# Optimization experiments

Hardware: AMD Instinct MI355X
Metric: run time of the kernel (lower is better)

The kernel has to match this reference:

```python
import jax, jax.numpy as jnp
import numpy as np


def conv2d(x, w, b=None):
    # 3x3, stride 1, pad 1, NCHW/OIHW
    y = jax.lax.conv_general_dilated(x, w, (1, 1), ((1, 1), (1, 1)),
                                     dimension_numbers=('NCHW', 'OIHW', 'NCHW'))
    return y if b is None else y + b[None, :, None, None]


def maxpool3s2(x):
    # MaxPool2d(kernel_size=3, stride=2, padding=1)
    return jax.lax.reduce_window(x, -jnp.inf, jax.lax.max,
                                 (1, 1, 3, 3), (1, 1, 2, 2),
                                 ((0, 0), (0, 0), (1, 1), (1, 1)))


def up2(x):
    # F.interpolate(scale_factor=2, mode='bilinear', align_corners=False)
    N, C, H, W = x.shape
    return jax.image.resize(x, (N, C, 2 * H, 2 * W), method='bilinear')


def deform_conv2d(x, offset, w, dg):
    # mmcv-style DeformConv2d (no modulation, no bias), 3x3, pad 1, stride 1.
    # offset: (N, dg*2*9, H, W) -> (N, dg, 9, (y,x), H, W)
    N, Cin, H, W = x.shape
    Cout = w.shape[0]
    K, pad = 9, 1
    Cg = Cin // dg
    off = offset.reshape(N, dg, K, 2, H, W)
    ky, kx = jnp.meshgrid(jnp.arange(3), jnp.arange(3), indexing='ij')
    kdy = (ky.reshape(K) - pad).astype(x.dtype)
    kdx = (kx.reshape(K) - pad).astype(x.dtype)
    gy = jnp.arange(H, dtype=x.dtype)
    gx = jnp.arange(W, dtype=x.dtype)
    py = off[:, :, :, 0] + gy[None, None, None, :, None] + kdy[None, None, :, None, None]
    px = off[:, :, :, 1] + gx[None, None, None, None, :] + kdx[None, None, :, None, None]
    y0f = jnp.floor(py)
    x0f = jnp.floor(px)
    wy = (py - y0f).reshape(N, dg, 1, K * H * W)
    wx = (px - x0f).reshape(N, dg, 1, K * H * W)
    y0 = y0f.astype(jnp.int32)
    x0 = x0f.astype(jnp.int32)
    xg = x.reshape(N, dg, Cg, H * W)

    def gather(yi, xi):
        valid = ((yi >= 0) & (yi < H) & (xi >= 0) & (xi < W))
        idx = (jnp.clip(yi, 0, H - 1) * W + jnp.clip(xi, 0, W - 1)).reshape(N, dg, 1, K * H * W)
        v = jnp.take_along_axis(xg, idx, axis=-1)  # (N, dg, Cg, K*H*W)
        return v * valid.reshape(N, dg, 1, K * H * W).astype(x.dtype)

    v00 = gather(y0, x0)
    v01 = gather(y0, x0 + 1)
    v10 = gather(y0 + 1, x0)
    v11 = gather(y0 + 1, x0 + 1)
    col = (v00 * (1 - wy) * (1 - wx) + v01 * (1 - wy) * wx
           + v10 * wy * (1 - wx) + v11 * wy * wx)
    col = col.reshape(N, Cin, K, H, W)  # im2col with bilinear sampling
    return jnp.einsum('ock,nckhw->nohw', w.reshape(Cout, Cin, K), col)


def pyramid(img, blocks):
    feats = []
    x = img
    for w1, b1, w2, b2 in blocks:
        x = jax.nn.relu(conv2d(x, w1, b1))
        x = jax.nn.relu(conv2d(x, w2, b2))
        x = maxpool3s2(x)
        feats.append(x)
    return feats


def _forward(ref_image, unreg_image,
             fe0_w1, fe0_b1, fe0_w2, fe0_b2,
             fe1_w1, fe1_b1, fe1_w2, fe1_b2,
             fe2_w1, fe2_b1, fe2_w2, fe2_b2,
             ob0_w, ob0_b, ob1_w, ob1_b, ob2_w, ob2_b,
             og0_w, og0_b, og1_w, og1_b, og2_w, og2_b,
             dc0_w, dc1_w, dc2_w,
             fc0_w, fc0_b, fc1_w, fc1_b, fc2_w, fc2_b,
             dob_w, dob_b, dog_w, dog_b, ddc_w):
    relu = jax.nn.relu
    blocks = [(fe0_w1, fe0_b1, fe0_w2, fe0_b2),
              (fe1_w1, fe1_b1, fe1_w2, fe1_b2),
              (fe2_w1, fe2_b1, fe2_w2, fe2_b2)]
    rf = pyramid(ref_image, blocks)
    uf = pyramid(unreg_image, blocks)
    ob = [(ob0_w, ob0_b), (ob1_w, ob1_b), (ob2_w, ob2_b)]
    og = [(og0_w, og0_b), (og1_w, og1_b), (og2_w, og2_b)]
    dc = [dc0_w, dc1_w, dc2_w]
    fc = [(fc0_w, fc0_b), (fc1_w, fc1_b), (fc2_w, fc2_b)]
    offs = [None] * 3
    feats = [None] * 3
    for i in range(2, -1, -1):  # coarse to fine
        o = relu(conv2d(jnp.concatenate([rf[i], uf[i]], axis=1), *ob[i]))
        inp = o if i == 2 else jnp.concatenate([o, up2(offs[i + 1])], axis=1)
        offs[i] = relu(conv2d(inp, *og[i]))  # 18-channel offsets
        f = relu(deform_conv2d(uf[i], offs[i], dc[i], 1))
        finp = f if i == 2 else jnp.concatenate([f, up2(feats[i + 1])], axis=1)
        feats[i] = relu(conv2d(finp, *fc[i]))
    do = conv2d(jnp.concatenate([rf[0], feats[0]], axis=1), dob_w, dob_b)
    do = conv2d(jnp.concatenate([do, offs[0]], axis=1), dog_w, dog_b)  # 36-ch offsets
    return deform_conv2d(feats[0], do, ddc_w, 2)  # (N, 2, H/2, W/2)


def setup_inputs() -> dict:
    key = jax.random.key(0)
    ks = iter(jax.random.split(key, 48))
    IC = 16

    def W(cout, cin):
        return jax.random.normal(next(ks), (cout, cin, 3, 3), jnp.float32) / np.sqrt(cin * 9.0)

    def B(c):
        return jax.random.normal(next(ks), (c,), jnp.float32) * 0.01

    d = {
        'ref_image': jax.random.normal(next(ks), (4, 1, 512, 512), jnp.float32),
        'unreg_image': jax.random.normal(next(ks), (4, 1, 512, 512), jnp.float32),
        'fe0_w1': W(IC, 1), 'fe0_b1': B(IC), 'fe0_w2': W(IC, IC), 'fe0_b2': B(IC),
        'fe1_w1': W(IC, IC), 'fe1_b1': B(IC), 'fe1_w2': W(IC, IC), 'fe1_b2': B(IC),
        'fe2_w1': W(IC, IC), 'fe2_b1': B(IC), 'fe2_w2': W(IC, IC), 'fe2_b2': B(IC),
        'ob0_w': W(IC, 2 * IC), 'ob0_b': B(IC),
        'ob1_w': W(IC, 2 * IC), 'ob1_b': B(IC),
        'ob2_w': W(IC, 2 * IC), 'ob2_b': B(IC),
        'og0_w': W(18, IC + 18), 'og0_b': B(18),
        'og1_w': W(18, IC + 18), 'og1_b': B(18),
        'og2_w': W(18, IC), 'og2_b': B(18),
        'dc0_w': W(IC, IC), 'dc1_w': W(IC, IC), 'dc2_w': W(IC, IC),
        'fc0_w': W(IC, 2 * IC), 'fc0_b': B(IC),
        'fc1_w': W(IC, 2 * IC), 'fc1_b': B(IC),
        'fc2_w': W(IC, IC), 'fc2_b': B(IC),
        'dob_w': W(IC, 2 * IC), 'dob_b': B(IC),
        'dog_w': W(36, IC + 18), 'dog_b': B(36),
        'ddc_w': W(2, IC),
    }
    return d


def reference(ref_image, unreg_image,
              fe0_w1, fe0_b1, fe0_w2, fe0_b2,
              fe1_w1, fe1_b1, fe1_w2, fe1_b2,
              fe2_w1, fe2_b1, fe2_w2, fe2_b2,
              ob0_w, ob0_b, ob1_w, ob1_b, ob2_w, ob2_b,
              og0_w, og0_b, og1_w, og1_b, og2_w, og2_b,
              dc0_w, dc1_w, dc2_w,
              fc0_w, fc0_b, fc1_w, fc1_b, fc2_w, fc2_b,
              dob_w, dob_b, dog_w, dog_b, ddc_w):
    return _forward(ref_image, unreg_image,
                    fe0_w1, fe0_b1, fe0_w2, fe0_b2,
                    fe1_w1, fe1_b1, fe1_w2, fe1_b2,
                    fe2_w1, fe2_b1, fe2_w2, fe2_b2,
                    ob0_w, ob0_b, ob1_w, ob1_b, ob2_w, ob2_b,
                    og0_w, og0_b, og1_w, og1_b, og2_w, og2_b,
                    dc0_w, dc1_w, dc2_w,
                    fc0_w, fc0_b, fc1_w, fc1_b, fc2_w, fc2_b,
                    dob_w, dob_b, dog_w, dog_b, ddc_w)
```

## Files before the change

kernel.cpp:

```cpp
#include <hip/hip_runtime.h>
#include <math.h>

typedef _Float16 half2_t __attribute__((ext_vector_type(2)));
typedef _Float16 half8 __attribute__((ext_vector_type(8)));
typedef float floatx4 __attribute__((ext_vector_type(4)));

__device__ __forceinline__ unsigned packh2(float a, float b) {
  half2_t h;
  h.x = (_Float16)a;
  h.y = (_Float16)b;
  return __builtin_bit_cast(unsigned, h);
}
__device__ __forceinline__ unsigned short f2h(float a) {
  return __builtin_bit_cast(unsigned short, (_Float16)a);
}
__device__ __forceinline__ float h2f(unsigned short u) {
  return (float)__builtin_bit_cast(_Float16, u);
}
__device__ __forceinline__ float dot2acc(unsigned a, unsigned b, float c) {
  half2_t ha = __builtin_bit_cast(half2_t, a);
  half2_t hb = __builtin_bit_cast(half2_t, b);
#if __has_builtin(__builtin_amdgcn_fdot2)
  return __builtin_amdgcn_fdot2(ha, hb, c, false);
#else
  c = fmaf((float)ha.x, (float)hb.x, c);
  return fmaf((float)ha.y, (float)hb.y, c);
#endif
}
__device__ __forceinline__ half8 splat8(_Float16 x) {
  half8 r;
#pragma unroll
  for (int j = 0; j < 8; ++j) r[j] = x;
  return r;
}

__global__ __launch_bounds__(256) void wdcpair_k(
    const float* __restrict__ a, const float* __restrict__ b,
    const float* __restrict__ c, const float* __restrict__ d,
    unsigned* __restrict__ out) {
  int t = blockIdx.x * 256 + threadIdx.x;
  if (t < 3456) {
    int conv = t / 1152, r = t % 1152;
    int k = r / 128, cp = (r / 16) % 8, o = r & 15;
    const float* w = conv == 0 ? a : (conv == 1 ? b : c);
    out[t] = packh2(w[(o * 16 + 2 * cp) * 9 + k], w[(o * 16 + 2 * cp + 1) * 9 + k]);
  } else if (t < 3600) {
    int r = t - 3456;
    int o = r & 1, jp = (r >> 1) & 3, g = (r >> 3) & 1, k = r >> 4;
    out[t] = packh2(d[(o * 16 + g * 8 + 2 * jp) * 9 + k],
                    d[(o * 16 + g * 8 + 2 * jp + 1) * 9 + k]);
  }
}

__global__ __launch_bounds__(256) void wmfma_k(
    const float* __restrict__ w0, const float* __restrict__ w1,
    const float* __restrict__ w2, const float* __restrict__ w3,
    const float* __restrict__ w4, const float* __restrict__ w5,
    unsigned short* __restrict__ out) {
  int t = blockIdx.x * 256 + threadIdx.x;
  if (t >= 15360) return;
  int conv = t / 2560, r = t % 2560;
  int c = r / 512, L = (r / 8) % 64, j = r & 7;
  int quad = L >> 4, o = L & 15;
  int k = 32 * c + quad * 8 + j;
  int tap = k >> 4, cin = k & 15;
  float v;
  if (conv == 5) {
    v = (tap < 9 && cin == 0) ? w5[o * 9 + tap] : 0.f;
  } else {
    const float* w = conv == 0 ? w0 : conv == 1 ? w1 : conv == 2 ? w2 : conv == 3 ? w3 : w4;
    v = (tap < 9) ? w[((size_t)o * 16 + cin) * 9 + tap] : 0.f;
  }
  out[t] = f2h(v);
}

struct W32Entry { const float* src; int cin; };
struct W32Table { W32Entry e[8]; };
__global__ __launch_bounds__(256) void wmfma32_k(W32Table t, unsigned short* __restrict__ out) {
  int i = blockIdx.x * 256 + threadIdx.x;
  if (i >= 7 * 4608) return;
  int conv = i / 4608, r = i % 4608;
  int tap = r / 512, L = (r / 8) % 64, j = r & 7;
  int quad = L >> 4, o = L & 15;
  int c = quad * 8 + j;
  W32Entry en = t.e[conv];
  float v = (c < en.cin) ? en.src[((size_t)o * en.cin + c) * 9 + tap] : 0.f;
  out[i] = f2h(v);
}

struct SPEntry { const float* src; int cin; int cout; int ct; int dstoff; };
struct SPTable { SPEntry e[4]; };
__global__ __launch_bounds__(256) void wsplit_k(SPTable t, unsigned short* __restrict__ out) {
  SPEntry en = t.e[blockIdx.y];
  int aSize = en.ct * 2560;
  int bSize = (en.cin > 16) ? en.ct * 4608 : 0;
  int i = blockIdx.x * 256 + threadIdx.x;
  if (i >= aSize + bSize) return;
  float v;
  if (i < aSize) {
    int ct = i / 2560, r = i % 2560;
    int c = r / 512, L = (r / 8) % 64, j = r & 7;
    int quad = L >> 4, o16 = L & 15;
    int k = 32 * c + quad * 8 + j;
    int tap = k >> 4, cin = k & 15;
    int o = ct * 16 + o16;
    v = (tap < 9 && o < en.cout) ? en.src[((size_t)o * en.cin + cin) * 9 + tap] : 0.f;
  } else {
    int r2 = i - aSize;
    int ct = r2 / 4608, r = r2 % 4608;
    int tap = r / 512, L = (r / 8) % 64, j = r & 7;
    int quad = L >> 4, o16 = L & 15;
    int cin = quad * 8 + j;
    int o = ct * 16 + o16;
    v = (cin < en.cin - 16 && o < en.cout)
            ? en.src[((size_t)o * en.cin + 16 + cin) * 9 + tap] : 0.f;
  }
  out[en.dstoff + i] = f2h(v);
}

__device__ __forceinline__ void conv_mfma(
    const unsigned short* __restrict__ src, int SW,
    unsigned short* __restrict__ dst, int DPS, const half8* __restrict__ bf,
    const float* __restrict__ bias, int POS, int OW, int tid, int relu,
    int domask, int gby, int gbx, int bound) {
  const int lane = tid & 63, wid = tid >> 6;
  const int quad = lane >> 4, m = lane & 15;
  const int tap01 = quad >> 1, cin8 = (quad & 1) * 8;
  const int ntiles = (POS + 15) >> 4;
  float bs = bias[m];
  half8 zero;
#pragma unroll
  for (int j = 0; j < 8; ++j) zero[j] = (_Float16)0;
  for (int T = wid; T < ntiles; T += 4) {
    int pa = T * 16 + m;
    pa = pa < POS ? pa : POS - 1;
    int ya = pa / OW, xa = pa - ya * OW;
    floatx4 acc = {0.f, 0.f, 0.f, 0.f};
#pragma unroll
    for (int c = 0; c < 5; ++c) {
      int tap = 2 * c + tap01;
      half8 a = zero;
      if (tap < 9) {
        int dy = tap / 3, dx = tap - (tap / 3) * 3;
        a = *(const half8*)(src + ((ya + dy) * SW + xa + dx) * 16 + cin8);
      }
      acc = __builtin_amdgcn_mfma_f32_16x16x32_f16(a, bf[c], acc, 0, 0, 0);
    }
#pragma unroll
    for (int r = 0; r < 4; ++r) {
      int pd = T * 16 + quad * 4 + r;
      if (pd < POS) {
        float v = acc[r] + bs;
        if (relu) v = fmaxf(v, 0.f);
        if (domask) {
          int yd = pd / OW, xd = pd - (pd / OW) * OW;
          int gy = gby + yd, gx = gbx + xd;
          if (gy < 0 || gy >= bound || gx < 0 || gx >= bound) v = 0.f;
        }
        dst[pd * DPS + m] = f2h(v);
      }
    }
  }
}

__device__ __forceinline__ void conv_mfma32(
    const unsigned short* __restrict__ src, int SW,
    unsigned short* __restrict__ dst, int DPS, const half8* __restrict__ bf,
    const float* __restrict__ bias, int POS, int OW, int tid, int relu,
    int domask, int gby, int gbx, int bound) {
  const int lane = tid & 63, wid = tid >> 6;
  const int quad = lane >> 4, m = lane & 15;
  const int ntiles = (POS + 15) >> 4;
  float bs = bias[m];
  for (int T = wid; T < ntiles; T += 4) {
    int pa = T * 16 + m;
    pa = pa < POS ? pa : POS - 1;
    int ya = pa / OW, xa = pa - ya * OW;
    floatx4 acc = {0.f, 0.f, 0.f, 0.f};
#pragma unroll
    for (int tap = 0; tap < 9; ++tap) {
      int dy = tap / 3, dx = tap - (tap / 3) * 3;
      half8 a = *(const half8*)(src + ((ya + dy) * SW + xa + dx) * 32 + quad * 8);
      acc = __builtin_amdgcn_mfma_f32_16x16x32_f16(a, bf[tap], acc, 0, 0, 0);
    }
#pragma unroll
    for (int r = 0; r < 4; ++r) {
      int pd = T * 16 + quad * 4 + r;
      if (pd < POS) {
        float v = acc[r] + bs;
        if (relu) v = fmaxf(v, 0.f);
        if (domask) {
          int yd = pd / OW, xd = pd - (pd / OW) * OW;
          int gy = gby + yd, gx = gbx + xd;
          if (gy < 0 || gy >= bound || gx < 0 || gx >= bound) v = 0.f;
        }
        dst[pd * DPS + m] = f2h(v);
      }
    }
  }
}

template <int CT, int HASB, int NT>
__device__ __forceinline__ void conv_split_mfma(
    const unsigned short* __restrict__ srcB, const unsigned short* __restrict__ srcO,
    const unsigned short* __restrict__ wbase, float* __restrict__ outLds, int OSTRIDE,
    const float* __restrict__ bias, int NOUT, int relu, int tid) {
  const int lane = tid & 63, wid = tid >> 6;
  const int quad = lane >> 4, m = lane & 15;
  const int tap01 = quad >> 1, cin8 = (quad & 1) * 8;
  half8 zero;
#pragma unroll
  for (int j = 0; j < 8; ++j) zero[j] = (_Float16)0;
  floatx4 acc[CT][NT];
#pragma unroll
  for (int ct = 0; ct < CT; ++ct)
#pragma unroll
    for (int t = 0; t < NT; ++t) acc[ct][t] = floatx4{0.f, 0.f, 0.f, 0.f};
#pragma unroll
  for (int ct = 0; ct < CT; ++ct) {
    half8 bfA[5];
#pragma unroll
    for (int c = 0; c < 5; ++c)
      bfA[c] = *(const half8*)(wbase + ((ct * 5 + c) * 64 + lane) * 8);
#pragma unroll
    for (int t = 0; t < NT; ++t) {
      int pa = (wid + 4 * t) * 16 + m;
      int ya = pa >> 4, xa = pa & 15;
#pragma unroll
      for (int c = 0; c < 5; ++c) {
        int tap = 2 * c + tap01;
        half8 a = zero;
        if (tap < 9) {
          int dy = tap / 3, dx = tap - (tap / 3) * 3;
          a = *(const half8*)(srcB + ((ya + dy) * 18 + xa + dx) * 18 + cin8);
        }
        acc[ct][t] = __builtin_amdgcn_mfma_f32_16x16x32_f16(a, bfA[c], acc[ct][t], 0, 0, 0);
      }
    }
  }
  if (HASB) {
    const unsigned short* wb = wbase + CT * 2560;
#pragma unroll
    for (int ct = 0; ct < CT; ++ct) {
      half8 bfB[9];
#pragma unroll
      for (int c = 0; c < 9; ++c)
        bfB[c] = *(const half8*)(wb + ((ct * 9 + c) * 64 + lane) * 8);
#pragma unroll
      for (int t = 0; t < NT; ++t) {
        int pa = (wid + 4 * t) * 16 + m;
        int ya = pa >> 4, xa = pa & 15;
#pragma unroll
        for (int tap = 0; tap < 9; ++tap) {
          int dy = tap / 3, dx = tap - (tap / 3) * 3;
          half8 a = *(const half8*)(srcO + ((ya + dy) * 18 + xa + dx) * 34 + quad * 8);
          acc[ct][t] = __builtin_amdgcn_mfma_f32_16x16x32_f16(a, bfB[tap], acc[ct][t], 0, 0, 0);
        }
      }
    }
  }
  __syncthreads();
#pragma unroll
  for (int ct = 0; ct < CT; ++ct) {
    int o = ct * 16 + m;
#pragma unroll
    for (int t = 0; t < NT; ++t) {
#pragma unroll
      for (int r = 0; r < 4; ++r) {
        int pd = (wid + 4 * t) * 16 + quad * 4 + r;
        if (o < NOUT) {
          float v = acc[ct][t][r] + bias[o];
          if (relu) v = fmaxf(v, 0.f);
          outLds[pd * OSTRIDE + o] = v;
        }
      }
    }
  }
}

__global__ __launch_bounds__(256) void fe0_fused_k(
    const float* __restrict__ refI, const float* __restrict__ unrI,
    const unsigned short* __restrict__ wm1, const float* __restrict__ b1,
    const unsigned short* __restrict__ wm2, const float* __restrict__ b2,
    float* __restrict__ outR, float* __restrict__ outU,
    unsigned short* __restrict__ outRH, unsigned short* __restrict__ outUH) {
  __shared__ __attribute__((aligned(16))) unsigned short bufA[441 * 16];
  __shared__ __attribute__((aligned(16))) unsigned short c1h[361 * 16];
  const int z = blockIdx.z;
  const int im = z >> 2, n = z & 3;
  const float* img = (im ? unrI : refI) + (size_t)n * 512 * 512;
  float* outp = (im ? outU : outR) + (size_t)n * 16 * 256 * 256;
  unsigned short* outh = (im ? outUH : outRH) + (size_t)n * 256 * 256 * 16;
  const int py0 = blockIdx.y * 8, px0 = blockIdx.x * 8;
  const int tid = threadIdx.x;

  half8 bf1[5], bf2[5];
  {
    const int lane = tid & 63;
#pragma unroll
    for (int c = 0; c < 5; ++c) {
      bf1[c] = *(const half8*)(wm1 + (c * 64 + lane) * 8);
      bf2[c] = *(const half8*)(wm2 + (c * 64 + lane) * 8);
    }
  }

  {
    unsigned* s32 = (unsigned*)bufA;
    for (int i = tid; i < 441; i += 256) {
      int yi = i / 21, xi = i - yi * 21;
      int gy = 2 * py0 - 3 + yi, gx = 2 * px0 - 3 + xi;
      float v = 0.f;
      if (gy >= 0 && gy < 512 && gx >= 0 && gx < 512) v = img[gy * 512 + gx];
      uint4 q0 = {packh2(v, 0.f), 0u, 0u, 0u};
      uint4 q1 = {0u, 0u, 0u, 0u};
      *(uint4*)(s32 + i * 8) = q0;
      *(uint4*)(s32 + i * 8 + 4) = q1;
    }
  }
  __syncthreads();

  conv_mfma(bufA, 21, c1h, 16, bf1, b1, 361, 19, tid, 1, 1, 2 * py0 - 2, 2 * px0 - 2, 512);
  __syncthreads();
  conv_mfma(c1h, 19, bufA, 18, bf2, b2, 289, 17, tid, 1, 0, 0, 0, 0);
  __syncthreads();

  unsigned short* stage = c1h;
  for (int i = tid; i < 1024; i += 256) {
    int c = i & 15, r = i >> 4;
    int py = r >> 3, px = r & 7;
    unsigned short m = 0;
#pragma unroll
    for (int dy = 0; dy < 3; ++dy) {
      int gy = 2 * (py0 + py) - 1 + dy;
      if (gy < 0 || gy >= 512) continue;
#pragma unroll
      for (int dx = 0; dx < 3; ++dx) {
        int gx = 2 * (px0 + px) - 1 + dx;
        if (gx < 0 || gx >= 512) continue;
        unsigned short v = bufA[((2 * py + dy) * 17 + 2 * px + dx) * 18 + c];
        m = (v > m) ? v : m;
      }
    }
    stage[r * 18 + c] = m;
  }
  __syncthreads();

  for (int i = tid; i < 1024; i += 256) {
    int c = i >> 6, r = i & 63, py = r >> 3, px = r & 7;
    unsigned short hb = stage[r * 18 + c];
    outp[((size_t)c * 256 + py0 + py) * 256 + px0 + px] = h2f(hb);
    outh[(((size_t)(py0 + py)) * 256 + px0 + px) * 16 + c] = hb;
  }
}

__global__ __launch_bounds__(256) void fe12_fused_k(
    const float* __restrict__ in,
    const unsigned short* __restrict__ wm1, const float* __restrict__ b1,
    const unsigned short* __restrict__ wm2, const float* __restrict__ b2,
    float* __restrict__ outC, unsigned short* __restrict__ outHWC, int Hin) {
  __shared__ __attribute__((aligned(16))) unsigned short inh[441 * 16];
  __shared__ __attribute__((aligned(16))) unsigned short c1h[361 * 16];
  const int n = blockIdx.z;
  const int Ho = Hin >> 1;
  const int py0 = blockIdx.y * 8, px0 = blockIdx.x * 8;
  const int tid = threadIdx.x;
  const float* inN = in + (size_t)n * 16 * Hin * Hin;
  const size_t HH = (size_t)Hin * Hin;

  half8 bf1[5], bf2[5];
  {
    const int lane = tid & 63;
#pragma unroll
    for (int c = 0; c < 5; ++c) {
      bf1[c] = *(const half8*)(wm1 + (c * 64 + lane) * 8);
      bf2[c] = *(const half8*)(wm2 + (c * 64 + lane) * 8);
    }
  }

  unsigned* inh32 = (unsigned*)inh;
  for (int i = tid; i < 8 * 441; i += 256) {
    int cp = i / 441, r = i - cp * 441;
    int yi = r / 21, xi = r - yi * 21;
    int gy = 2 * py0 - 3 + yi, gx = 2 * px0 - 3 + xi;
    float v0 = 0.f, v1 = 0.f;
    if (gy >= 0 && gy < Hin && gx >= 0 && gx < Hin) {
      const float* s = inN + (size_t)(2 * cp) * HH + (size_t)gy * Hin + gx;
      v0 = s[0];
      v1 = s[HH];
    }
    inh32[r * 8 + cp] = packh2(v0, v1);
  }
  __syncthreads();

  conv_mfma(inh, 21, c1h, 16, bf1, b1, 361, 19, tid, 1, 1, 2 * py0 - 2, 2 * px0 - 2, Hin);
  __syncthreads();
  conv_mfma(c1h, 19, inh, 18, bf2, b2, 289, 17, tid, 1, 0, 0, 0, 0);
  __syncthreads();

  unsigned short* stage = c1h;
  for (int i = tid; i < 1024; i += 256) {
    int c = i & 15, r = i >> 4;
    int py = r >> 3, px = r & 7;
    unsigned short m = 0;
#pragma unroll
    for (int dy = 0; dy < 3; ++dy) {
      int gy = 2 * (py0 + py) - 1 + dy;
      if (gy < 0 || gy >= Hin) continue;
#pragma unroll
      for (int dx = 0; dx < 3; ++dx) {
        int gx = 2 * (px0 + px) - 1 + dx;
        if (gx < 0 || gx >= Hin) continue;
        unsigned short v = inh[((2 * py + dy) * 17 + 2 * px + dx) * 18 + c];
        m = (v > m) ? v : m;
      }
    }
    stage[r * 18 + c] = m;
  }
  __syncthreads();

  float* outp = outC + (size_t)n * 16 * Ho * Ho;
  for (int i = tid; i < 1024; i += 256) {
    int c = i >> 6, r = i & 63, py = r >> 3, px = r & 7;
    unsigned short hb = stage[r * 18 + c];
    outp[((size_t)c * Ho + py0 + py) * Ho + px0 + px] = h2f(hb);
    if (n >= 4)
      outHWC[(((size_t)(n - 4) * Ho + py0 + py) * Ho + px0 + px) * 16 + c] = hb;
  }
}

template <int HAS_UP>
__global__ __launch_bounds__(256) void obog_k(
    const float* __restrict__ rf, const float* __restrict__ uf,
    const unsigned short* __restrict__ offsUp,
    const unsigned short* __restrict__ wmob, const float* __restrict__ bob,
    const unsigned short* __restrict__ wog, const float* __restrict__ bog,
    unsigned short* __restrict__ offsOut, int H) {
  __shared__ __attribute__((aligned(16))) unsigned POOL[5460];
  const int n = blockIdx.z;
  const int bx = blockIdx.x * 16, by = blockIdx.y * 8;
  const int tid = threadIdx.x;
  const size_t HH = (size_t)H * H;
  const float* r0 = rf + (size_t)n * 16 * HH;
  const float* u0 = uf + (size_t)n * 16 * HH;

  for (int i = tid; i < 3840; i += 256) {
    int cp = i / 240, r = i - cp * 240;
    int ly = r / 20, lx = r - ly * 20;
    int gy = by + ly - 2, gx = bx + lx - 2;
    float v0 = 0.f, v1 = 0.f;
    if (gy >= 0 && gy < H && gx >= 0 && gx < H) {
      const float* s = (cp < 8) ? r0 + (size_t)(2 * cp) * HH : u0 + (size_t)(2 * cp - 16) * HH;
      size_t off = (size_t)gy * H + gx;
      v0 = s[off];
      v1 = s[HH + off];
    }
    POOL[r * 16 + cp] = packh2(v0, v1);
  }
  __syncthreads();

  {
    half8 bf[9];
    const int lane = tid & 63;
#pragma unroll
    for (int c = 0; c < 9; ++c) bf[c] = *(const half8*)(wmob + (c * 64 + lane) * 8);
    conv_mfma32((const unsigned short*)POOL, 20, (unsigned short*)(POOL + 3840), 18,
                bf, bob, 180, 18, tid, 1, 1, by - 1, bx - 1, H);
  }
  __syncthreads();

  if (HAS_UP) {
    const int H2 = H >> 1;
    const unsigned short* os = offsUp + (size_t)n * 18 * H2 * H2;
    for (int i = tid; i < 16 * 180; i += 256) {
      int cp = i / 180, r = i - cp * 180;
      unsigned val = 0u;
      if (cp < 9) {
        int y1 = r / 18, x1 = r - y1 * 18;
        int gy = by + y1 - 1, gx = bx + x1 - 1;
        if (gy >= 0 && gy < H && gx >= 0 && gx < H) {
          float sy = 0.5f * gy - 0.25f, sx = 0.5f * gx - 0.25f;
          float y0f = floorf(sy), x0f = floorf(sx);
          float wy = sy - y0f, wx = sx - x0f;
          int y0 = (int)y0f, x0 = (int)x0f;
          int y0c = min(max(y0, 0), H2 - 1), y1c = min(max(y0 + 1, 0), H2 - 1);
          int x0c = min(max(x0, 0), H2 - 1), x1c = min(max(x0 + 1, 0), H2 - 1);
          const unsigned short* sp = os + (size_t)(2 * cp) * H2 * H2;
          float v0 = (1.f - wy) * ((1.f - wx) * h2f(sp[y0c * H2 + x0c]) + wx * h2f(sp[y0c * H2 + x1c])) +
                     wy * ((1.f - wx) * h2f(sp[y1c * H2 + x0c]) + wx * h2f(sp[y1c * H2 + x1c]));
          sp += (size_t)H2 * H2;
          float v1 = (1.f - wy) * ((1.f - wx) * h2f(sp[y0c * H2 + x0c]) + wx * h2f(sp[y0c * H2 + x1c])) +
                     wy * ((1.f - wx) * h2f(sp[y1c * H2 + x0c]) + wx * h2f(sp[y1c * H2 + x1c]));
          val = packh2(v0, v1);
        }
      }
      POOL[r * 17 + cp] = val;
    }
    __syncthreads();
  }

  conv_split_mfma<2, HAS_UP, 2>((const unsigned short*)(POOL + 3840),
                                (const unsigned short*)POOL, wog,
                                (float*)POOL, 19, bog, 18, 1, tid);
  __syncthreads();

  {
    int pix = tid & 127, half = tid >> 7;
    const float* of = (const float*)POOL + (size_t)pix * 19 + half * 9;
    int ty = pix >> 4, tx = pix & 15;
    unsigned short* op = offsOut + (size_t)n * 18 * HH + (size_t)(half * 9) * HH +
                         (size_t)(by + ty) * H + (bx + tx);
#pragma unroll
    for (int o = 0; o < 9; ++o) op[(size_t)o * HH] = f2h(of[o]);
  }
}

template <int HAS_UP>
__global__ __launch_bounds__(256) void defc_k(
    const unsigned short* __restrict__ ufHWC, const unsigned short* __restrict__ offs,
    const unsigned* __restrict__ wdc2, const float* __restrict__ featsUp,
    const unsigned short* __restrict__ wmfc, const float* __restrict__ bfc,
    float* __restrict__ featsOut, unsigned short* __restrict__ outHwc, int H) {
  __shared__ __attribute__((aligned(16))) unsigned ldsC[180 * 17];
  const int n = blockIdx.z;
  const int bx = blockIdx.x * 16, by = blockIdx.y * 8;
  const int tid = threadIdx.x;
  const size_t HH = (size_t)H * H;
  const unsigned short* inN = ufHWC + (size_t)n * HH * 16;
  const unsigned short* offN = offs + (size_t)n * 18 * HH;

  half8 bf[9];
  {
    const int lane = tid & 63;
#pragma unroll
    for (int c = 0; c < 9; ++c) bf[c] = *(const half8*)(wmfc + (c * 64 + lane) * 8);
  }

  for (int p = tid; p < 180; p += 256) {
    int y1 = p / 18, x1 = p - y1 * 18;
    int h = by + y1 - 1, w = bx + x1 - 1;
    bool valid = (h >= 0 && h < H && w >= 0 && w < H);
    float acc[16];
#pragma unroll
    for (int o = 0; o < 16; ++o) acc[o] = 0.f;
    if (valid) {
      size_t hw = (size_t)h * H + w;
#pragma unroll
      for (int k = 0; k < 9; ++k) {
        int ky = k / 3 - 1, kx = k % 3 - 1;
        float oy = h2f(offN[(size_t)(2 * k) * HH + hw]);
        float ox = h2f(offN[(size_t)(2 * k + 1) * HH + hw]);
        float py = (float)(h + ky) + oy;
        float px = (float)(w + kx) + ox;
        float y0f = floorf(py), x0f = floorf(px);
        float fy = py - y0f, fx = px - x0f;
        int y0 = (int)y0f, x0 = (int)x0f;
        bool vy0 = ((unsigned)y0 < (unsigned)H);
        bool vy1 = ((unsigned)(y0 + 1) < (unsigned)H);
        bool vx0 = ((unsigned)x0 < (unsigned)H);
        bool vx1 = ((unsigned)(x0 + 1) < (unsigned)H);
        int y0c = min(max(y0, 0), H - 1), y1c = min(max(y0 + 1, 0), H - 1);
        int x0c = min(max(x0, 0), H - 1), x1c = min(max(x0 + 1, 0), H - 1);
        float w00 = (vy0 && vx0) ? (1.f - fy) * (1.f - fx) : 0.f;
        float w01 = (vy0 && vx1) ? (1.f - fy) * fx : 0.f;
        float w10 = (vy1 && vx0) ? fy * (1.f - fx) : 0.f;
        float w11 = (vy1 && vx1) ? fy * fx : 0.f;
        half8 s00 = splat8((_Float16)w00);
        half8 s01 = splat8((_Float16)w01);
        half8 s10 = splat8((_Float16)w10);
        half8 s11 = splat8((_Float16)w11);
        const unsigned short* p00 = inN + ((size_t)y0c * H + x0c) * 16;
        const unsigned short* p01 = inN + ((size_t)y0c * H + x1c) * 16;
        const unsigned short* p10 = inN + ((size_t)y1c * H + x0c) * 16;
        const unsigned short* p11 = inN + ((size_t)y1c * H + x1c) * 16;
        const unsigned* wk2 = wdc2 + k * 128;
#pragma unroll
        for (int c8 = 0; c8 < 2; ++c8) {
          half8 a00 = *(const half8*)(p00 + c8 * 8);
          half8 a01 = *(const half8*)(p01 + c8 * 8);
          half8 a10 = *(const half8*)(p10 + c8 * 8);
          half8 a11 = *(const half8*)(p11 + c8 * 8);
          half8 vb = a00 * s00 + a01 * s01 + a10 * s10 + a11 * s11;
          uint4 vp = __builtin_bit_cast(uint4, vb);
          unsigned vpa[4] = {vp.x, vp.y, vp.z, vp.w};
#pragma unroll
          for (int jp = 0; jp < 4; ++jp) {
            const unsigned* wrow = wk2 + (c8 * 4 + jp) * 16;
#pragma unroll
            for (int o = 0; o < 16; ++o)
              acc[o] = dot2acc(vpa[jp], wrow[o], acc[o]);
          }
        }
      }
    }
#pragma unroll
    for (int cc = 0; cc < 8; ++cc) {
      float a0 = valid ? fmaxf(acc[2 * cc], 0.f) : 0.f;
      float a1 = valid ? fmaxf(acc[2 * cc + 1], 0.f) : 0.f;
      ldsC[p * 17 + cc] = packh2(a0, a1);
      if (!HAS_UP) ldsC[p * 17 + 8 + cc] = 0u;
    }
  }

  if (HAS_UP) {
    const int H2 = H >> 1;
    const float* fu = featsUp + (size_t)n * 16 * H2 * H2;
    for (int i = tid; i < 8 * 180; i += 256) {
      int cp = i / 180, r = i - cp * 180;
      int y1 = r / 18, x1 = r - y1 * 18;
      int gy = by + y1 - 1, gx = bx + x1 - 1;
      float v0 = 0.f, v1 = 0.f;
      if (gy >= 0 && gy < H && gx >= 0 && gx < H) {
        float sy = 0.5f * gy - 0.25f, sx = 0.5f * gx - 0.25f;
        float y0f = floorf(sy), x0f = floorf(sx);
        float wy = sy - y0f, wx = sx - x0f;
        int y0 = (int)y0f, x0 = (int)x0f;
        int y0c = min(max(y0, 0), H2 - 1), y1c = min(max(y0 + 1, 0), H2 - 1);
        int x0c = min(max(x0, 0), H2 - 1), x1c = min(max(x0 + 1, 0), H2 - 1);
        const float* sp = fu + (size_t)(2 * cp) * H2 * H2;
        v0 = (1.f - wy) * ((1.f - wx) * sp[y0c * H2 + x0c] + wx * sp[y0c * H2 + x1c]) +
             wy * ((1.f - wx) * sp[y1c * H2 + x0c] + wx * sp[y1c * H2 + x1c]);
        sp += (size_t)H2 * H2;
        v1 = (1.f - wy) * ((1.f - wx) * sp[y0c * H2 + x0c] + wx * sp[y0c * H2 + x1c]) +
             wy * ((1.f - wx) * sp[y1c * H2 + x0c] + wx * sp[y1c * H2 + x1c]);
      }
      ldsC[r * 17 + 8 + cp] = packh2(v0, v1);
    }
  }
  __syncthreads();

  {
    const int lane = tid & 63, wid = tid >> 6;
    const int quad = lane >> 4, m = lane & 15;
    const unsigned short* src = (const unsigned short*)ldsC;
    float bs = bfc[m];
    for (int T = wid; T < 8; T += 4) {
      int pa = T * 16 + m;
      int ya = pa >> 4, xa = pa & 15;
      floatx4 acc = {0.f, 0.f, 0.f, 0.f};
#pragma unroll
      for (int tap = 0; tap < 9; ++tap) {
        int dy = tap / 3, dx = tap - (tap / 3) * 3;
        half8 a = *(const half8*)(src + ((ya + dy) * 18 + xa + dx) * 34 + quad * 8);
        acc = __builtin_amdgcn_mfma_f32_16x16x32_f16(a, bf[tap], acc, 0, 0, 0);
      }
#pragma unroll
      for (int r = 0; r < 4; ++r) {
        int pd = T * 16 + quad * 4 + r;
        int yd = pd >> 4, xd = pd & 15;
        float v = fmaxf(acc[r] + bs, 0.f);
        if (featsOut)
          featsOut[(size_t)n * 16 * HH + (size_t)m * HH + (size_t)(by + yd) * H + bx + xd] = v;
        if (outHwc)
          outHwc[((size_t)n * HH + (size_t)(by + yd) * H + bx + xd) * 16 + m] = f2h(v);
      }
    }
  }
}

__global__ __launch_bounds__(256) void final_k(
    const unsigned short* __restrict__ rfh, const unsigned short* __restrict__ f0hwc,
    const unsigned short* __restrict__ offs0,
    const unsigned short* __restrict__ wmdob, const float* __restrict__ bdob,
    const unsigned short* __restrict__ wdog, const float* __restrict__ bdog,
    const unsigned* __restrict__ wddc2, float* __restrict__ out) {
  __shared__ __attribute__((aligned(16))) unsigned POOL[9472];
  const int H = 256;
  const size_t HH = 65536;
  const int n = blockIdx.z;
  const int bx = blockIdx.x * 16, by = blockIdx.y * 16;
  const int tid = threadIdx.x;
  const unsigned short* r0h = rfh + (size_t)n * HH * 16;
  const unsigned short* f0h = f0hwc + (size_t)n * HH * 16;

  for (int i = tid; i < 6400; i += 256) {
    int cp = i / 400, r = i - cp * 400;
    int ly = r / 20, lx = r - ly * 20;
    int gy = by + ly - 2, gx = bx + lx - 2;
    unsigned val = 0u;
    if (gy >= 0 && gy < H && gx >= 0 && gx < H) {
      const unsigned short* base = (cp < 8) ? r0h : f0h;
      int ch = (cp < 8) ? 2 * cp : 2 * cp - 16;
      val = *(const unsigned*)(base + ((size_t)gy * H + gx) * 16 + ch);
    }
    POOL[r * 16 + cp] = val;
  }
  __syncthreads();

  {
    half8 bf[9];
    const int lane = tid & 63;
#pragma unroll
    for (int c = 0; c < 9; ++c) bf[c] = *(const half8*)(wmdob + (c * 64 + lane) * 8);
    conv_mfma32((const unsigned short*)POOL, 20, (unsigned short*)(POOL + 6400), 18,
                bf, bdob, 324, 18, tid, 0, 1, by - 1, bx - 1, H);
  }
  __syncthreads();

  {
    const unsigned short* os = offs0 + (size_t)n * 18 * HH;
    for (int i = tid; i < 16 * 324; i += 256) {
      int cp = i / 324, r = i - cp * 324;
      unsigned val = 0u;
      if (cp < 9) {
        int y1 = r / 18, x1 = r - y1 * 18;
        int gy = by + y1 - 1, gx = bx + x1 - 1;
        if (gy >= 0 && gy < H && gx >= 0 && gx < H) {
          const unsigned short* s = os + (size_t)(2 * cp) * HH + (size_t)gy * H + gx;
          val = (unsigned)s[0] | ((unsigned)s[HH] << 16);
        }
      }
      POOL[r * 17 + cp] = val;
    }
    __syncthreads();
  }

  conv_split_mfma<3, 1, 4>((const unsigned short*)(POOL + 6400),
                           (const unsigned short*)POOL, wdog,
                           (float*)POOL, 37, bdog, 36, 0, tid);
  __syncthreads();

  {
    const int ty = tid >> 4, tx = tid & 15;
    const int h = by + ty, w = bx + tx;
    const float* a36 = (const float*)POOL + (size_t)tid * 37;
    float rr[2] = {0.f, 0.f};
#pragma unroll
    for (int g = 0; g < 2; ++g) {
#pragma unroll
      for (int k = 0; k < 9; ++k) {
        int ky = k / 3 - 1, kx = k % 3 - 1;
        float oy = a36[(g * 9 + k) * 2 + 0];
        float ox = a36[(g * 9 + k) * 2 + 1];
        float py = (float)(h + ky) + oy;
        float px = (float)(w + kx) + ox;
        float y0f = floorf(py), x0f = floorf(px);
        float fy = py - y0f, fx = px - x0f;
        int y0 = (int)y0f, x0 = (int)x0f;
        bool vy0 = ((unsigned)y0 < (unsigned)H);
        bool vy1 = ((unsigned)(y0 + 1) < (unsigned)H);
        bool vx0 = ((unsigned)x0 < (unsigned)H);
        bool vx1 = ((unsigned)(x0 + 1) < (unsigned)H);
        int y0c = min(max(y0, 0), H - 1), y1c = min(max(y0 + 1, 0), H - 1);
        int x0c = min(max(x0, 0), H - 1), x1c = min(max(x0 + 1, 0), H - 1);
        float w00 = (vy0 && vx0) ? (1.f - fy) * (1.f - fx) : 0.f;
        float w01 = (vy0 && vx1) ? (1.f - fy) * fx : 0.f;
        float w10 = (vy1 && vx0) ? fy * (1.f - fx) : 0.f;
        float w11 = (vy1 && vx1) ? fy * fx : 0.f;
        half8 s00 = splat8((_Float16)w00);
        half8 s01 = splat8((_Float16)w01);
        half8 s10 = splat8((_Float16)w10);
        half8 s11 = splat8((_Float16)w11);
        const unsigned short* p00 = f0h + ((size_t)y0c * H + x0c) * 16 + g * 8;
        const unsigned short* p01 = f0h + ((size_t)y0c * H + x1c) * 16 + g * 8;
        const unsigned short* p10 = f0h + ((size_t)y1c * H + x0c) * 16 + g * 8;
        const unsigned short* p11 = f0h + ((size_t)y1c * H + x1c) * 16 + g * 8;
        half8 a00 = *(const half8*)p00;
        half8 a01 = *(const half8*)p01;
        half8 a10 = *(const half8*)p10;
        half8 a11 = *(const half8*)p11;
        half8 vb = a00 * s00 + a01 * s01 + a10 * s10 + a11 * s11;
        uint4 vp = __builtin_bit_cast(uint4, vb);
        unsigned vpa[4] = {vp.x, vp.y, vp.z, vp.w};
        const unsigned* wk2 = wddc2 + ((size_t)k * 2 + g) * 8;
#pragma unroll
        for (int jp = 0; jp < 4; ++jp) {
          rr[0] = dot2acc(vpa[jp], wk2[jp * 2 + 0], rr[0]);
          rr[1] = dot2acc(vpa[jp], wk2[jp * 2 + 1], rr[1]);
        }
      }
    }
    out[((size_t)n * 2 + 0) * HH + (size_t)h * H + w] = rr[0];
    out[((size_t)n * 2 + 1) * HH + (size_t)h * H + w] = rr[1];
  }
}

extern "C" void kernel_launch(void* const* d_in, const int* in_sizes, int n_in,
                              void* d_out, int out_size, void* d_ws, size_t ws_size,
                              hipStream_t stream) {
  auto F = [&](int i) { return (const float*)d_in[i]; };
  const float* ref = F(0);
  const float* unr = F(1);
  const float* few1[3] = {F(2), F(6), F(10)};
  const float* feb1[3] = {F(3), F(7), F(11)};
  const float* few2[3] = {F(4), F(8), F(12)};
  const float* feb2[3] = {F(5), F(9), F(13)};
  const float* obw[3] = {F(14), F(16), F(18)};
  const float* obb[3] = {F(15), F(17), F(19)};
  const float* ogw[3] = {F(20), F(22), F(24)};
  const float* ogb[3] = {F(21), F(23), F(25)};
  const float* dcw[3] = {F(26), F(27), F(28)};
  const float* fcw[3] = {F(29), F(31), F(33)};
  const float* fcb[3] = {F(30), F(32), F(34)};
  const float* dobw = F(35);
  const float* dobb = F(36);
  const float* dogw = F(37);
  const float* dogb = F(38);
  const float* ddcw = F(39);

  float* ws = (float*)d_ws;
  size_t p = 0;
  auto alloc = [&](size_t nf) { float* r = ws + p; p += nf; return r; };
  float* rf0 = alloc((size_t)4 * 16 * 65536);
  float* uf0 = alloc((size_t)4 * 16 * 65536);
  float* rf1 = alloc((size_t)4 * 16 * 16384);
  float* uf1 = alloc((size_t)4 * 16 * 16384);
  float* rf2 = alloc((size_t)4 * 16 * 4096);
  float* uf2 = alloc((size_t)4 * 16 * 4096);
  unsigned short* offs0 = (unsigned short*)alloc((size_t)4 * 18 * 65536 / 2);
  unsigned short* offs1 = (unsigned short*)alloc((size_t)4 * 18 * 16384 / 2);
  unsigned short* offs2 = (unsigned short*)alloc((size_t)4 * 18 * 4096 / 2);
  float* feats1 = alloc((size_t)4 * 16 * 16384);
  float* feats2 = alloc((size_t)4 * 16 * 4096);
  unsigned short* rfH0 = (unsigned short*)alloc((size_t)4 * 16 * 65536 / 2);
  unsigned short* ufH0 = (unsigned short*)alloc((size_t)4 * 16 * 65536 / 2);
  unsigned short* ufH1 = (unsigned short*)alloc((size_t)4 * 16 * 16384 / 2);
  unsigned short* ufH2 = (unsigned short*)alloc((size_t)4 * 16 * 4096 / 2);
  unsigned short* fHwc = (unsigned short*)alloc((size_t)4 * 16 * 65536 / 2);
  float* wdc2f = alloc(3600);
  float* wmf = alloc(7680);
  float* wm32f = alloc(16200);
  float* wspl = alloc(27648);
  if (p * sizeof(float) > ws_size) return;
  unsigned* wdc2 = (unsigned*)wdc2f;
  unsigned short* wmh = (unsigned short*)wmf;
  unsigned short* wm32 = (unsigned short*)wm32f;
  unsigned short* wsp = (unsigned short*)wspl;

  W32Table T32;
  T32.e[0] = {obw[0], 32}; T32.e[1] = {obw[1], 32}; T32.e[2] = {obw[2], 32};
  T32.e[3] = {dobw, 32};   T32.e[4] = {fcw[0], 32}; T32.e[5] = {fcw[1], 32};
  T32.e[6] = {fcw[2], 16};
  auto o32 = [](int i) { return i * 4608; };

  SPTable TS;
  TS.e[0] = {ogw[0], 34, 18, 2, 0};
  TS.e[1] = {ogw[1], 34, 18, 2, 14336};
  TS.e[2] = {ogw[2], 16, 18, 2, 28672};
  TS.e[3] = {dogw, 34, 36, 3, 33792};
  const int o_og[3] = {0, 14336, 28672};
  const int o_dog = 33792;

  wdcpair_k<<<15, 256, 0, stream>>>(dcw[0], dcw[1], dcw[2], ddcw, wdc2);
  wmfma_k<<<60, 256, 0, stream>>>(few2[0], few1[1], few2[1], few1[2], few2[2],
                                  few1[0], wmh);
  wmfma32_k<<<126, 256, 0, stream>>>(T32, wm32);
  wsplit_k<<<dim3(84, 4), 256, 0, stream>>>(TS, wsp);

  fe0_fused_k<<<dim3(32, 32, 8), 256, 0, stream>>>(
      ref, unr, wmh + 5 * 2560, feb1[0], wmh, feb2[0], rf0, uf0, rfH0, ufH0);
  fe12_fused_k<<<dim3(16, 16, 8), 256, 0, stream>>>(
      rf0, wmh + 2560, feb1[1], wmh + 2 * 2560, feb2[1], rf1, ufH1, 256);
  fe12_fused_k<<<dim3(8, 8, 8), 256, 0, stream>>>(
      rf1, wmh + 3 * 2560, feb1[2], wmh + 4 * 2560, feb2[2], rf2, ufH2, 128);

  obog_k<0><<<dim3(4, 8, 4), 256, 0, stream>>>(
      rf2, uf2, nullptr, wm32 + o32(2), obb[2], wsp + o_og[2], ogb[2], offs2, 64);
  defc_k<0><<<dim3(4, 8, 4), 256, 0, stream>>>(
      ufH2, offs2, wdc2 + 2 * 1152, nullptr, wm32 + o32(6), fcb[2], feats2, nullptr, 64);
  obog_k<1><<<dim3(8, 16, 4), 256, 0, stream>>>(
      rf1, uf1, offs2, wm32 + o32(1), obb[1], wsp + o_og[1], ogb[1], offs1, 128);
  defc_k<1><<<dim3(8, 16, 4), 256, 0, stream>>>(
      ufH1, offs1, wdc2 + 1 * 1152, feats2, wm32 + o32(5), fcb[1], feats1, nullptr, 128);
  obog_k<1><<<dim3(16, 32, 4), 256, 0, stream>>>(
      rf0, uf0, offs1, wm32 + o32(0), obb[0], wsp + o_og[0], ogb[0], offs0, 256);
  defc_k<1><<<dim3(16, 32, 4), 256, 0, stream>>>(
      ufH0, offs0, wdc2, feats1, wm32 + o32(4), fcb[0], nullptr, fHwc, 256);

  final_k<<<dim3(16, 16, 4), 256, 0, stream>>>(
      rfH0, fHwc, offs0, wm32 + o32(3), dobb, wsp + o_dog, dogb, wdc2 + 3456,
      (float*)d_out);
}
```

Measured before the change: 540.8 us.

## Store all intermediate feature maps only as fp16 HWC and drop fp32 NCHW copies

Feature-extractor, offset and fusion kernels now write and read a single fp16 channel-interleaved (HWC) buffer instead of both an fp32 NCHW copy and an fp16 HWC copy. Loads become one 32-bit read per channel pair instead of two strided fp32 reads, and the LDS staging pass and barrier before the output write are removed. This cuts global write and read traffic across the whole pipeline. In exchange, upsampling interpolation now reads fp16 inputs, and the direct HWC stores from the pooling loop are 2-byte scattered writes.

```diff
diff --git a/kernel.cpp b/kernel.cpp
--- a/kernel.cpp
+++ b/kernel.cpp
@@ -282,15 +282,13 @@
     const float* __restrict__ refI, const float* __restrict__ unrI,
     const unsigned short* __restrict__ wm1, const float* __restrict__ b1,
     const unsigned short* __restrict__ wm2, const float* __restrict__ b2,
-    float* __restrict__ outR, float* __restrict__ outU,
-    unsigned short* __restrict__ outRH, unsigned short* __restrict__ outUH) {
+    unsigned short* __restrict__ outH) {
   __shared__ __attribute__((aligned(16))) unsigned short bufA[441 * 16];
   __shared__ __attribute__((aligned(16))) unsigned short c1h[361 * 16];
   const int z = blockIdx.z;
   const int im = z >> 2, n = z & 3;
   const float* img = (im ? unrI : refI) + (size_t)n * 512 * 512;
-  float* outp = (im ? outU : outR) + (size_t)n * 16 * 256 * 256;
-  unsigned short* outh = (im ? outUH : outRH) + (size_t)n * 256 * 256 * 16;
+  unsigned short* outh = outH + (size_t)z * 65536 * 16;
   const int py0 = blockIdx.y * 8, px0 = blockIdx.x * 8;
   const int tid = threadIdx.x;
 
@@ -324,7 +322,6 @@
   conv_mfma(c1h, 19, bufA, 18, bf2, b2, 289, 17, tid, 1, 0, 0, 0, 0);
   __syncthreads();
 
-  unsigned short* stage = c1h;
   for (int i = tid; i < 1024; i += 256) {
     int c = i & 15, r = i >> 4;
     int py = r >> 3, px = r & 7;
@@ -341,31 +338,22 @@
         m = (v > m) ? v : m;
       }
     }
-    stage[r * 18 + c] = m;
-  }
-  __syncthreads();
-
-  for (int i = tid; i < 1024; i += 256) {
-    int c = i >> 6, r = i & 63, py = r >> 3, px = r & 7;
-    unsigned short hb = stage[r * 18 + c];
-    outp[((size_t)c * 256 + py0 + py) * 256 + px0 + px] = h2f(hb);
-    outh[(((size_t)(py0 + py)) * 256 + px0 + px) * 16 + c] = hb;
+    outh[(((size_t)(py0 + py)) * 256 + px0 + px) * 16 + c] = m;
   }
 }
 
 __global__ __launch_bounds__(256) void fe12_fused_k(
-    const float* __restrict__ in,
+    const unsigned short* __restrict__ inH,
     const unsigned short* __restrict__ wm1, const float* __restrict__ b1,
     const unsigned short* __restrict__ wm2, const float* __restrict__ b2,
-    float* __restrict__ outC, unsigned short* __restrict__ outHWC, int Hin) {
+    unsigned short* __restrict__ outH, int Hin) {
   __shared__ __attribute__((aligned(16))) unsigned short inh[441 * 16];
   __shared__ __attribute__((aligned(16))) unsigned short c1h[361 * 16];
   const int n = blockIdx.z;
   const int Ho = Hin >> 1;
   const int py0 = blockIdx.y * 8, px0 = blockIdx.x * 8;
   const int tid = threadIdx.x;
-  const float* inN = in + (size_t)n * 16 * Hin * Hin;
-  const size_t HH = (size_t)Hin * Hin;
+  const unsigned short* inN = inH + (size_t)n * Hin * Hin * 16;
 
   half8 bf1[5], bf2[5];
   {
@@ -382,13 +370,10 @@
     int cp = i / 441, r = i - cp * 441;
     int yi = r / 21, xi = r - yi * 21;
     int gy = 2 * py0 - 3 + yi, gx = 2 * px0 - 3 + xi;
-    float v0 = 0.f, v1 = 0.f;
-    if (gy >= 0 && gy < Hin && gx >= 0 && gx < Hin) {
-      const float* s = inN + (size_t)(2 * cp) * HH + (size_t)gy * Hin + gx;
-      v0 = s[0];
-      v1 = s[HH];
-    }
-    inh32[r * 8 + cp] = packh2(v0, v1);
+    unsigned val = 0u;
+    if (gy >= 0 && gy < Hin && gx >= 0 && gx < Hin)
+      val = *(const unsigned*)(inN + ((size_t)gy * Hin + gx) * 16 + 2 * cp);
+    inh32[r * 8 + cp] = val;
   }
   __syncthreads();
 
@@ -397,7 +382,7 @@
   conv_mfma(c1h, 19, inh, 18, bf2, b2, 289, 17, tid, 1, 0, 0, 0, 0);
   __syncthreads();
 
-  unsigned short* stage = c1h;
+  unsigned short* outp = outH + (size_t)n * Ho * Ho * 16;
   for (int i = tid; i < 1024; i += 256) {
     int c = i & 15, r = i >> 4;
     int py = r >> 3, px = r & 7;
@@ -414,23 +399,13 @@
         m = (v > m) ? v : m;
       }
     }
-    stage[r * 18 + c] = m;
-  }
-  __syncthreads();
-
-  float* outp = outC + (size_t)n * 16 * Ho * Ho;
-  for (int i = tid; i < 1024; i += 256) {
-    int c = i >> 6, r = i & 63, py = r >> 3, px = r & 7;
-    unsigned short hb = stage[r * 18 + c];
-    outp[((size_t)c * Ho + py0 + py) * Ho + px0 + px] = h2f(hb);
-    if (n >= 4)
-      outHWC[(((size_t)(n - 4) * Ho + py0 + py) * Ho + px0 + px) * 16 + c] = hb;
+    outp[(((size_t)(py0 + py)) * Ho + px0 + px) * 16 + c] = m;
   }
 }
 
 template <int HAS_UP>
 __global__ __launch_bounds__(256) void obog_k(
-    const float* __restrict__ rf, const float* __restrict__ uf,
+    const unsigned short* __restrict__ rfh, const unsigned short* __restrict__ ufh,
     const unsigned short* __restrict__ offsUp,
     const unsigned short* __restrict__ wmob, const float* __restrict__ bob,
     const unsigned short* __restrict__ wog, const float* __restrict__ bog,
@@ -440,21 +415,20 @@
   const int bx = blockIdx.x * 16, by = blockIdx.y * 8;
   const int tid = threadIdx.x;
   const size_t HH = (size_t)H * H;
-  const float* r0 = rf + (size_t)n * 16 * HH;
-  const float* u0 = uf + (size_t)n * 16 * HH;
+  const unsigned short* r0h = rfh + (size_t)n * HH * 16;
+  const unsigned short* u0h = ufh + (size_t)n * HH * 16;
 
   for (int i = tid; i < 3840; i += 256) {
     int cp = i / 240, r = i - cp * 240;
     int ly = r / 20, lx = r - ly * 20;
     int gy = by + ly - 2, gx = bx + lx - 2;
-    float v0 = 0.f, v1 = 0.f;
+    unsigned val = 0u;
     if (gy >= 0 && gy < H && gx >= 0 && gx < H) {
-      const float* s = (cp < 8) ? r0 + (size_t)(2 * cp) * HH : u0 + (size_t)(2 * cp - 16) * HH;
-      size_t off = (size_t)gy * H + gx;
-      v0 = s[off];
-      v1 = s[HH + off];
-    }
-    POOL[r * 16 + cp] = packh2(v0, v1);
+      const unsigned short* s16 = (cp < 8) ? r0h : u0h;
+      int ch = (cp < 8) ? 2 * cp : 2 * cp - 16;
+      val = *(const unsigned*)(s16 + ((size_t)gy * H + gx) * 16 + ch);
+    }
+    POOL[r * 16 + cp] = val;
   }
   __syncthreads();
 
@@ -517,9 +491,9 @@
 template <int HAS_UP>
 __global__ __launch_bounds__(256) void defc_k(
     const unsigned short* __restrict__ ufHWC, const unsigned short* __restrict__ offs,
-    const unsigned* __restrict__ wdc2, const float* __restrict__ featsUp,
+    const unsigned* __restrict__ wdc2, const unsigned short* __restrict__ featsUpH,
     const unsigned short* __restrict__ wmfc, const float* __restrict__ bfc,
-    float* __restrict__ featsOut, unsigned short* __restrict__ outHwc, int H) {
+    unsigned short* __restrict__ outHwc, int H) {
   __shared__ __attribute__((aligned(16))) unsigned ldsC[180 * 17];
   const int n = blockIdx.z;
   const int bx = blockIdx.x * 16, by = blockIdx.y * 8;
@@ -603,12 +577,12 @@
 
   if (HAS_UP) {
     const int H2 = H >> 1;
-    const float* fu = featsUp + (size_t)n * 16 * H2 * H2;
+    const unsigned short* fu = featsUpH + (size_t)n * H2 * H2 * 16;
     for (int i = tid; i < 8 * 180; i += 256) {
       int cp = i / 180, r = i - cp * 180;
       int y1 = r / 18, x1 = r - y1 * 18;
       int gy = by + y1 - 1, gx = bx + x1 - 1;
-      float v0 = 0.f, v1 = 0.f;
+      unsigned val = 0u;
       if (gy >= 0 && gy < H && gx >= 0 && gx < H) {
         float sy = 0.5f * gy - 0.25f, sx = 0.5f * gx - 0.25f;
         float y0f = floorf(sy), x0f = floorf(sx);
@@ -616,14 +590,17 @@
         int y0 = (int)y0f, x0 = (int)x0f;
         int y0c = min(max(y0, 0), H2 - 1), y1c = min(max(y0 + 1, 0), H2 - 1);
         int x0c = min(max(x0, 0), H2 - 1), x1c = min(max(x0 + 1, 0), H2 - 1);
-        const float* sp = fu + (size_t)(2 * cp) * H2 * H2;
-        v0 = (1.f - wy) * ((1.f - wx) * sp[y0c * H2 + x0c] + wx * sp[y0c * H2 + x1c]) +
-             wy * ((1.f - wx) * sp[y1c * H2 + x0c] + wx * sp[y1c * H2 + x1c]);
-        sp += (size_t)H2 * H2;
-        v1 = (1.f - wy) * ((1.f - wx) * sp[y0c * H2 + x0c] + wx * sp[y0c * H2 + x1c]) +
-             wy * ((1.f - wx) * sp[y1c * H2 + x0c] + wx * sp[y1c * H2 + x1c]);
-      }
-      ldsC[r * 17 + 8 + cp] = packh2(v0, v1);
+        half2_t h00 = __builtin_bit_cast(half2_t, *(const unsigned*)(fu + ((size_t)y0c * H2 + x0c) * 16 + 2 * cp));
+        half2_t h01 = __builtin_bit_cast(half2_t, *(const unsigned*)(fu + ((size_t)y0c * H2 + x1c) * 16 + 2 * cp));
+        half2_t h10 = __builtin_bit_cast(half2_t, *(const unsigned*)(fu + ((size_t)y1c * H2 + x0c) * 16 + 2 * cp));
+        half2_t h11 = __builtin_bit_cast(half2_t, *(const unsigned*)(fu + ((size_t)y1c * H2 + x1c) * 16 + 2 * cp));
+        float v0 = (1.f - wy) * ((1.f - wx) * (float)h00.x + wx * (float)h01.x) +
+                   wy * ((1.f - wx) * (float)h10.x + wx * (float)h11.x);
+        float v1 = (1.f - wy) * ((1.f - wx) * (float)h00.y + wx * (float)h01.y) +
+                   wy * ((1.f - wx) * (float)h10.y + wx * (float)h11.y);
+        val = packh2(v0, v1);
+      }
+      ldsC[r * 17 + 8 + cp] = val;
     }
   }
   __syncthreads();
@@ -648,10 +625,7 @@
         int pd = T * 16 + quad * 4 + r;
         int yd = pd >> 4, xd = pd & 15;
         float v = fmaxf(acc[r] + bs, 0.f);
-        if (featsOut)
-          featsOut[(size_t)n * 16 * HH + (size_t)m * HH + (size_t)(by + yd) * H + bx + xd] = v;
-        if (outHwc)
-          outHwc[((size_t)n * HH + (size_t)(by + yd) * H + bx + xd) * 16 + m] = f2h(v);
+        outHwc[((size_t)n * HH + (size_t)(by + yd) * H + bx + xd) * 16 + m] = f2h(v);
       }
     }
   }
@@ -800,22 +774,15 @@
   float* ws = (float*)d_ws;
   size_t p = 0;
   auto alloc = [&](size_t nf) { float* r = ws + p; p += nf; return r; };
-  float* rf0 = alloc((size_t)4 * 16 * 65536);
-  float* uf0 = alloc((size_t)4 * 16 * 65536);
-  float* rf1 = alloc((size_t)4 * 16 * 16384);
-  float* uf1 = alloc((size_t)4 * 16 * 16384);
-  float* rf2 = alloc((size_t)4 * 16 * 4096);
-  float* uf2 = alloc((size_t)4 * 16 * 4096);
+  unsigned short* fH0 = (unsigned short*)alloc((size_t)8 * 16 * 65536 / 2);
+  unsigned short* fH1 = (unsigned short*)alloc((size_t)8 * 16 * 16384 / 2);
+  unsigned short* fH2 = (unsigned short*)alloc((size_t)8 * 16 * 4096 / 2);
+  unsigned short* ftH1 = (unsigned short*)alloc((size_t)4 * 16 * 16384 / 2);
+  unsigned short* ftH2 = (unsigned short*)alloc((size_t)4 * 16 * 4096 / 2);
+  unsigned short* fHwc = (unsigned short*)alloc((size_t)4 * 16 * 65536 / 2);
   unsigned short* offs0 = (unsigned short*)alloc((size_t)4 * 18 * 65536 / 2);
   unsigned short* offs1 = (unsigned short*)alloc((size_t)4 * 18 * 16384 / 2);
   unsigned short* offs2 = (unsigned short*)alloc((size_t)4 * 18 * 4096 / 2);
-  float* feats1 = alloc((size_t)4 * 16 * 16384);
-  float* feats2 = alloc((size_t)4 * 16 * 4096);
-  unsigned short* rfH0 = (unsigned short*)alloc((size_t)4 * 16 * 65536 / 2);
-  unsigned short* ufH0 = (unsigned short*)alloc((size_t)4 * 16 * 65536 / 2);
-  unsigned short* ufH1 = (unsigned short*)alloc((size_t)4 * 16 * 16384 / 2);
-  unsigned short* ufH2 = (unsigned short*)alloc((size_t)4 * 16 * 4096 / 2);
-  unsigned short* fHwc = (unsigned short*)alloc((size_t)4 * 16 * 65536 / 2);
   float* wdc2f = alloc(3600);
   float* wmf = alloc(7680);
   float* wm32f = alloc(16200);
@@ -847,26 +814,30 @@
   wsplit_k<<<dim3(84, 4), 256, 0, stream>>>(TS, wsp);
 
   fe0_fused_k<<<dim3(32, 32, 8), 256, 0, stream>>>(
-      ref, unr, wmh + 5 * 2560, feb1[0], wmh, feb2[0], rf0, uf0, rfH0, ufH0);
+      ref, unr, wmh + 5 * 2560, feb1[0], wmh, feb2[0], fH0);
   fe12_fused_k<<<dim3(16, 16, 8), 256, 0, stream>>>(
-      rf0, wmh + 2560, feb1[1], wmh + 2 * 2560, feb2[1], rf1, ufH1, 256);
+      fH0, wmh + 2560, feb1[1], wmh + 2 * 2560, feb2[1], fH1, 256);
   fe12_fused_k<<<dim3(8, 8, 8), 256, 0, stream>>>(
-      rf1, wmh + 3 * 2560, feb1[2], wmh + 4 * 2560, feb2[2], rf2, ufH2, 128);
+      fH1, wmh + 3 * 2560, feb1[2], wmh + 4 * 2560, feb2[2], fH2, 128);
+
+  const unsigned short* uH0 = fH0 + (size_t)4 * 65536 * 16;
+  const unsigned short* uH1 = fH1 + (size_t)4 * 16384 * 16;
+  const unsigned short* uH2 = fH2 + (size_t)4 * 4096 * 16;
 
   obog_k<0><<<dim3(4, 8, 4), 256, 0, stream>>>(
-      rf2, uf2, nullptr, wm32 + o32(2), obb[2], wsp + o_og[2], ogb[2], offs2, 64);
+      fH2, uH2, nullptr, wm32 + o32(2), obb[2], wsp + o_og[2], ogb[2], offs2, 64);
   defc_k<0><<<dim3(4, 8, 4), 256, 0, stream>>>(
-      ufH2, offs2, wdc2 + 2 * 1152, nullptr, wm32 + o32(6), fcb[2], feats2, nullptr, 64);
+      uH2, offs2, wdc2 + 2 * 1152, nullptr, wm32 + o32(6), fcb[2], ftH2, 64);
   obog_k<1><<<dim3(8, 16, 4), 256, 0, stream>>>(
-      rf1, uf1, offs2, wm32 + o32(1), obb[1], wsp + o_og[1], ogb[1], offs1, 128);
+      fH1, uH1, offs2, wm32 + o32(1), obb[1], wsp + o_og[1], ogb[1], offs1, 128);
   defc_k<1><<<dim3(8, 16, 4), 256, 0, stream>>>(
-      ufH1, offs1, wdc2 + 1 * 1152, feats2, wm32 + o32(5), fcb[1], feats1, nullptr, 128);
+      uH1, offs1, wdc2 + 1 * 1152, ftH2, wm32 + o32(5), fcb[1], ftH1, 128);
   obog_k<1><<<dim3(16, 32, 4), 256, 0, stream>>>(
-      rf0, uf0, offs1, wm32 + o32(0), obb[0], wsp + o_og[0], ogb[0], offs0, 256);
+      fH0, uH0, offs1, wm32 + o32(0), obb[0], wsp + o_og[0], ogb[0], offs0, 256);
   defc_k<1><<<dim3(16, 32, 4), 256, 0, stream>>>(
-      ufH0, offs0, wdc2, feats1, wm32 + o32(4), fcb[0], nullptr, fHwc, 256);
+      uH0, offs0, wdc2, ftH1, wm32 + o32(4), fcb[0], fHwc, 256);
 
   final_k<<<dim3(16, 16, 4), 256, 0, stream>>>(
-      rfH0, fHwc, offs0, wm32 + o32(3), dobb, wsp + o_dog, dogb, wdc2 + 3456,
+      fH0, fHwc, offs0, wm32 + o32(3), dobb, wsp + o_dog, dogb, wdc2 + 3456,
       (float*)d_out);
 }
```

After: 511.4 us. 1.06x faster.
